# Kernel optimization log

Hardware: AMD Instinct MI355X
Metric: run time of the kernel (lower is better)

## Reference

```python
import jax, jax.numpy as jnp
import numpy as np

WS = 2
D = 128  # hidden_dim per direction
SCALE_X = float(np.sqrt(2.0))  # rescale=True, highway_bias=0 -> sqrt(1+exp(0))


def sru_bidir(x, W, wc, b, k):
    """Bidirectional single-layer SRU (sru lib, layer_norm=False, rescale=True).
    x: (L, N, din). Returns (L, N, 2*D)."""
    L, N, _ = x.shape
    U = (x @ W).reshape(L, N, 2, D, k)  # (L,N,dir,D,k)
    vf, vr = wc.reshape(2, 2, D)  # each (dir, D)
    bf, br = b.reshape(2, 2, D)
    # time-reverse the backward direction so one scan handles both
    U = jnp.concatenate([U[:, :, :1], U[::-1, :, 1:]], axis=2)
    if k == 4:
        xprime = U[..., 3]
    else:
        xp = x.reshape(L, N, 2, D)
        xprime = jnp.concatenate([xp[:, :, :1], xp[::-1, :, 1:]], axis=2) * SCALE_X

    def step(c, inp):
        u0, u1, u2, xpt = inp  # each (N,2,D)
        f = jax.nn.sigmoid(u1 + vf * c + bf)
        c = f * c + (1.0 - f) * u0
        r = jax.nn.sigmoid(u2 + vr * c + br)
        h = r * c + (1.0 - r) * xpt
        return c, h

    c0 = jnp.zeros((N, 2, D), dtype=x.dtype)
    _, H = jax.lax.scan(step, c0, (U[..., 0], U[..., 1], U[..., 2], xprime))
    # un-reverse backward direction outputs
    H = jnp.concatenate([H[:, :, :1], H[::-1, :, 1:]], axis=2)
    return H.reshape(L, N, 2 * D)


def setup_inputs() -> dict:
    key = jax.random.key(0)
    ks = jax.random.split(key, 6)
    B, C, Himg, Wimg = 8, 3, 224, 224
    F = WS * WS * C  # 12
    inp = {
        "x": jax.random.normal(ks[0], (B, C, Himg, Wimg), jnp.float32),
        "W1": jax.random.normal(ks[1], (F, 2 * D * 4), jnp.float32) * (1.0 / np.sqrt(F)),
        "wc1": jax.random.normal(ks[2], (2 * 2 * D,), jnp.float32) * 0.1,
        "b1": jnp.zeros((2 * 2 * D,), jnp.float32),
        "W2": jax.random.normal(ks[3], (2 * D, 2 * D * 3), jnp.float32) * (1.0 / np.sqrt(2 * D)),
        "wc2": jax.random.normal(ks[4], (2 * 2 * D,), jnp.float32) * 0.1,
        "b2": jnp.zeros((2 * 2 * D,), jnp.float32),
    }
    return inp


def reference(x, W1, wc1, b1, W2, wc2, b2):
    B, C, Himg, Wimg = x.shape
    Hp, Wp = Himg // WS, Wimg // WS
    F = WS * WS * C
    # get_valid_patches: (B, Hp, Wp, C*ws*ws) with (C, wh, ww) flatten order
    p = x.reshape(B, C, Hp, WS, Wp, WS).transpose(0, 2, 4, 1, 3, 5).reshape(B, Hp, Wp, F)
    # input_array = patches.permute(2,0,3,1) -> (Hp, B, Wp, F)
    # apply_one_direction on firstVRNN: merge Hp into batch, scan over Wp
    a1 = p.transpose(1, 0, 2, 3).reshape(Hp * B, Wp, F).transpose(1, 0, 2)  # (Wp, Hp*B, F)
    h1 = sru_bidir(a1, W1, wc1, b1, k=4)  # (Wp, Hp*B, 2D)
    h1 = h1.transpose(1, 0, 2).reshape(Hp, B, Wp, 2 * D)
    # vertical_results = out.permute(2,1,0,3) -> (Wp, B, Hp, 2D)
    v = h1.transpose(2, 1, 0, 3)
    # second direction: merge Wp into batch, scan over Hp
    a2 = v.reshape(Wp * B, Hp, 2 * D).transpose(1, 0, 2)  # (Hp, Wp*B, 2D)
    h2 = sru_bidir(a2, W2, wc2, b2, k=3)  # (Hp, Wp*B, 2D)
    h2 = h2.transpose(1, 0, 2).reshape(Wp, B, Hp, 2 * D)
    # feature_map.permute(1,3,2,0) -> (B, 2D, Hp, Wp)
    return h2.transpose(1, 3, 2, 0)
```

## Files before the change

### kernel.cpp

```cpp
#include <hip/hip_runtime.h>
#include <hip/hip_bf16.h>

typedef unsigned short ushort_t;
typedef unsigned int uint_t;

typedef __bf16 bf16x8 __attribute__((ext_vector_type(8)));
typedef float f32x4 __attribute__((ext_vector_type(4)));

__device__ __forceinline__ float bf2f(ushort_t u) {
    return __uint_as_float(((uint_t)u) << 16);
}
__device__ __forceinline__ ushort_t f2bf(float f) {
    uint_t x = __float_as_uint(f);
    uint_t r = (x + 0x7FFFu + ((x >> 16) & 1u)) >> 16;
    return (ushort_t)r;
}
__device__ __forceinline__ float sigmoidf_fast(float x) {
    return 1.0f / (1.0f + __expf(-x));
}

__global__ __launch_bounds__(256) void permute_w2(const float* __restrict__ W2,
                                                  ushort_t* __restrict__ W2t) {
    int i = blockIdx.x * 256 + threadIdx.x;
    int np = i >> 8;
    int k  = i & 255;
    int kk  = np >> 8;
    int rem = np & 255;
    int dir = rem >> 7;
    int d   = rem & 127;
    int oc = dir * 384 + d * 3 + kk;
    W2t[np * 256 + k] = f2bf(W2[k * 768 + oc]);
}

__global__ __launch_bounds__(256) void scan1(const float* __restrict__ x,
                                             const float* __restrict__ W1,
                                             const float* __restrict__ wc1,
                                             const float* __restrict__ b1,
                                             ushort_t* __restrict__ H1) {
    __shared__ float patch[112 * 12];
    const int n1 = blockIdx.x;
    const int hp = n1 >> 3, b = n1 & 7;
    const int tid = threadIdx.x;

    for (int e = tid; e < 1344; e += 256) {
        int c = e / 448;
        int rem = e % 448;
        int wh = rem / 224;
        int pos = rem % 224;
        float v = x[((b * 3 + c) * 224 + (2 * hp + wh)) * 224 + pos];
        patch[(pos >> 1) * 12 + c * 4 + wh * 2 + (pos & 1)] = v;
    }

    float4 w[12];
    const float4* W1v = (const float4*)W1;
#pragma unroll
    for (int j = 0; j < 12; ++j) w[j] = W1v[j * 256 + tid];

    const float vf = wc1[tid],       vr = wc1[256 + tid];
    const float bfv = b1[tid],       brv = b1[256 + tid];
    const int dir = tid >> 7;

    __syncthreads();

    float cst = 0.0f;
    for (int t = 0; t < 112; ++t) {
        const int tt = dir ? (111 - t) : t;
        const float4* pp = (const float4*)(patch + tt * 12);
        float4 p0 = pp[0], p1 = pp[1], p2 = pp[2];
        float pj[12] = {p0.x, p0.y, p0.z, p0.w, p1.x, p1.y, p1.z, p1.w,
                        p2.x, p2.y, p2.z, p2.w};
        float u0 = 0.f, u1 = 0.f, u2 = 0.f, u3 = 0.f;
#pragma unroll
        for (int j = 0; j < 12; ++j) {
            float pv = pj[j];
            u0 = fmaf(w[j].x, pv, u0);
            u1 = fmaf(w[j].y, pv, u1);
            u2 = fmaf(w[j].z, pv, u2);
            u3 = fmaf(w[j].w, pv, u3);
        }
        float f = sigmoidf_fast(u1 + vf * cst + bfv);
        cst = f * cst + (1.0f - f) * u0;
        float r = sigmoidf_fast(u2 + vr * cst + brv);
        float h = r * cst + (1.0f - r) * u3;
        H1[((size_t)(hp * 112 + tt) * 8 + b) * 256 + tid] = f2bf(h);
    }
}

__global__ __launch_bounds__(256) void gemm2(const ushort_t* __restrict__ A,
                                             const ushort_t* __restrict__ Bt,
                                             ushort_t* __restrict__ Cc) {
    __shared__ ushort_t As[128 * 32];
    __shared__ ushort_t Bs[128 * 32];
    const int m0 = blockIdx.y * 128;
    const int n0 = blockIdx.x * 128;
    const int tid = threadIdx.x;
    const int w = tid >> 6, lane = tid & 63;
    const int wm = w >> 1, wn = w & 1;
    const int lr = lane >> 2;
    const int lc = (lane & 3) * 8;
    const int ln16 = lane & 15;
    const int k8 = (lane >> 4) * 8;

    f32x4 acc[4][4] = {};

    for (int kb = 0; kb < 256; kb += 32) {
        if (kb) __syncthreads();
#pragma unroll
        for (int q = 0; q < 2; ++q) {
            int r = w * 32 + q * 16;
            const ushort_t* gA = A + (size_t)(m0 + r + lr) * 256 + kb + lc;
            __builtin_amdgcn_global_load_lds(
                (const __attribute__((address_space(1))) uint_t*)gA,
                (__attribute__((address_space(3))) uint_t*)(As + r * 32), 16, 0, 0);
            const ushort_t* gB = Bt + (size_t)(n0 + r + lr) * 256 + kb + lc;
            __builtin_amdgcn_global_load_lds(
                (const __attribute__((address_space(1))) uint_t*)gB,
                (__attribute__((address_space(3))) uint_t*)(Bs + r * 32), 16, 0, 0);
        }
        __syncthreads();

        bf16x8 af[4], bf[4];
#pragma unroll
        for (int i = 0; i < 4; ++i) {
            int ra = wm * 64 + i * 16 + ln16;
            af[i] = *(const bf16x8*)(As + ra * 32 + k8);
            int rb = wn * 64 + i * 16 + ln16;
            bf[i] = *(const bf16x8*)(Bs + rb * 32 + k8);
        }
#pragma unroll
        for (int i = 0; i < 4; ++i)
#pragma unroll
            for (int j = 0; j < 4; ++j)
                acc[i][j] = __builtin_amdgcn_mfma_f32_16x16x32_bf16(
                    af[i], bf[j], acc[i][j], 0, 0, 0);
    }

    const int rq = (lane >> 4) * 4;
#pragma unroll
    for (int i = 0; i < 4; ++i)
#pragma unroll
        for (int j = 0; j < 4; ++j)
#pragma unroll
            for (int r = 0; r < 4; ++r) {
                int gm = m0 + wm * 64 + i * 16 + rq + r;
                int gn = n0 + wn * 64 + j * 16 + ln16;
                Cc[(size_t)gm * 768 + gn] = f2bf(acc[i][j][r]);
            }
}

__global__ __launch_bounds__(256) void scan2(const ushort_t* __restrict__ U2,
                                             const ushort_t* __restrict__ H1,
                                             const float* __restrict__ wc2,
                                             const float* __restrict__ b2,
                                             float* __restrict__ H2) {
    const int n2 = blockIdx.x;
    const int wp = n2 >> 3, b = n2 & 7;
    const int tid = threadIdx.x;
    const int dir = tid >> 7;
    const float vf = wc2[tid],  vr = wc2[256 + tid];
    const float bfv = b2[tid],  brv = b2[256 + tid];
    const float SCALE_X = 1.41421356237309515f;

    float cst = 0.0f;
    for (int t = 0; t < 112; ++t) {
        const int tt = dir ? (111 - t) : t;
        const size_t m = (size_t)(tt * 112 + wp) * 8 + b;
        const ushort_t* u = U2 + m * 768;
        float u0 = bf2f(u[tid]);
        float u1 = bf2f(u[256 + tid]);
        float u2 = bf2f(u[512 + tid]);
        float xp = bf2f(H1[m * 256 + tid]) * SCALE_X;
        float f = sigmoidf_fast(u1 + vf * cst + bfv);
        cst = f * cst + (1.0f - f) * u0;
        float r = sigmoidf_fast(u2 + vr * cst + brv);
        H2[m * 256 + tid] = r * cst + (1.0f - r) * xp;
    }
}

__global__ __launch_bounds__(256) void transpose_out(const float* __restrict__ H2,
                                                     float* __restrict__ out) {
    __shared__ float tile[112 * 65];
    const int bid = blockIdx.x;
    const int cchunk = bid & 3;
    const int hp = (bid >> 2) % 112;
    const int b = bid / (4 * 112);
    const int tid = threadIdx.x;
    const int ch0 = cchunk * 64;

    for (int i = tid; i < 112 * 64; i += 256) {
        int wp = i >> 6;
        int c = i & 63;
        tile[wp * 65 + c] = H2[((size_t)(hp * 112 + wp) * 8 + b) * 256 + ch0 + c];
    }
    __syncthreads();
    for (int i = tid; i < 64 * 112; i += 256) {
        int c = i / 112;
        int wp = i % 112;
        out[((size_t)(b * 256 + ch0 + c) * 112 + hp) * 112 + wp] = tile[wp * 65 + c];
    }
}

extern "C" void kernel_launch(void* const* d_in, const int* in_sizes, int n_in,
                              void* d_out, int out_size, void* d_ws, size_t ws_size,
                              hipStream_t stream) {
    const float* x   = (const float*)d_in[0];
    const float* W1  = (const float*)d_in[1];
    const float* wc1 = (const float*)d_in[2];
    const float* b1  = (const float*)d_in[3];
    const float* W2  = (const float*)d_in[4];
    const float* wc2 = (const float*)d_in[5];
    const float* b2  = (const float*)d_in[6];
    float* out = (float*)d_out;

    char* ws = (char*)d_ws;
    ushort_t* H1  = (ushort_t*)(ws);
    ushort_t* U2  = (ushort_t*)(ws + 51380224);
    ushort_t* W2t = (ushort_t*)(ws + 51380224 + 154140672);
    float*    H2  = (float*)(ws + 51380224 + 154140672 + 393216);

    permute_w2<<<768, 256, 0, stream>>>(W2, W2t);
    scan1<<<896, 256, 0, stream>>>(x, W1, wc1, b1, H1);
    gemm2<<<dim3(6, 784), 256, 0, stream>>>(H1, W2t, U2);
    scan2<<<896, 256, 0, stream>>>(U2, H1, wc2, b2, H2);
    transpose_out<<<8 * 112 * 4, 256, 0, stream>>>(H2, out);
}
```

Before: 381.0 us.

## Store GEMM outputs channel-planar so scan2 writes final layout directly

scan1 now writes H1 in batch-major order. gemm2 writes U2 into per-gate planes laid out (b, channel, position), and a new xp_plane kernel transposes the scaled H1 into a fourth plane. scan2 is remapped so each thread owns one (channel, wp) column and writes the final NCHW output directly, with a one-step prefetch. This removes the separate H2 buffer and the transpose_out pass. The cost is an extra transpose kernel, scattered 8-byte stores from the GEMM epilogue, and many scan2 lanes idle because 112 of 128 wp slots are used.

```diff
diff --git a/kernel.cpp b/kernel.cpp
--- a/kernel.cpp
+++ b/kernel.cpp
@@ -18,6 +18,9 @@
 __device__ __forceinline__ float sigmoidf_fast(float x) {
     return 1.0f / (1.0f + __expf(-x));
 }
+
+#define PP 12544
+#define PLANE 25690112ULL
 
 __global__ __launch_bounds__(256) void permute_w2(const float* __restrict__ W2,
                                                   ushort_t* __restrict__ W2t) {
@@ -36,7 +39,7 @@
                                              const float* __restrict__ W1,
                                              const float* __restrict__ wc1,
                                              const float* __restrict__ b1,
-                                             ushort_t* __restrict__ H1) {
+                                             ushort_t* __restrict__ H1a) {
     __shared__ float patch[112 * 12];
     const int n1 = blockIdx.x;
     const int hp = n1 >> 3, b = n1 & 7;
@@ -82,17 +85,50 @@
         cst = f * cst + (1.0f - f) * u0;
         float r = sigmoidf_fast(u2 + vr * cst + brv);
         float h = r * cst + (1.0f - r) * u3;
-        H1[((size_t)(hp * 112 + tt) * 8 + b) * 256 + tid] = f2bf(h);
+        H1a[((size_t)b * PP + hp * 112 + tt) * 256 + tid] = f2bf(h);
+    }
+}
+
+__global__ __launch_bounds__(256) void xp_plane(const ushort_t* __restrict__ H1a,
+                                                ushort_t* __restrict__ U2t) {
+    __shared__ ushort_t tile[64 * 66];
+    const int pt = blockIdx.x;
+    const int ct = blockIdx.y;
+    const int b  = blockIdx.z;
+    const int p0 = pt * 64, ch0 = ct * 64;
+    const int tid = threadIdx.x;
+    const float SCALE_X = 1.41421356237309515f;
+
+#pragma unroll
+    for (int rep = 0; rep < 16; ++rep) {
+        int idx = rep * 256 + tid;
+        int pl = idx >> 6;
+        int cl = idx & 63;
+        float v = bf2f(H1a[((size_t)b * PP + p0 + pl) * 256 + ch0 + cl]);
+        tile[pl * 66 + cl] = f2bf(v * SCALE_X);
+    }
+    __syncthreads();
+#pragma unroll
+    for (int rep = 0; rep < 16; ++rep) {
+        int idx = rep * 256 + tid;
+        int cl = idx >> 6;
+        int pl = idx & 63;
+        U2t[3 * PLANE + ((size_t)b * 256 + ch0 + cl) * PP + p0 + pl] =
+            tile[pl * 66 + cl];
     }
 }
 
 __global__ __launch_bounds__(256) void gemm2(const ushort_t* __restrict__ A,
                                              const ushort_t* __restrict__ Bt,
-                                             ushort_t* __restrict__ Cc) {
+                                             ushort_t* __restrict__ U2t) {
     __shared__ ushort_t As[128 * 32];
     __shared__ ushort_t Bs[128 * 32];
     const int m0 = blockIdx.y * 128;
+    const int bb = blockIdx.y / 98;
+    const int p0 = (blockIdx.y % 98) * 128;
     const int n0 = blockIdx.x * 128;
+    const int kidx = n0 >> 8;
+    const int ch0  = n0 & 255;
     const int tid = threadIdx.x;
     const int w = tid >> 6, lane = tid & 63;
     const int wm = w >> 1, wn = w & 1;
@@ -122,10 +158,8 @@
         bf16x8 af[4], bf[4];
 #pragma unroll
         for (int i = 0; i < 4; ++i) {
-            int ra = wm * 64 + i * 16 + ln16;
-            af[i] = *(const bf16x8*)(As + ra * 32 + k8);
-            int rb = wn * 64 + i * 16 + ln16;
-            bf[i] = *(const bf16x8*)(Bs + rb * 32 + k8);
+            af[i] = *(const bf16x8*)(As + (wm * 64 + i * 16 + ln16) * 32 + k8);
+            bf[i] = *(const bf16x8*)(Bs + (wn * 64 + i * 16 + ln16) * 32 + k8);
         }
 #pragma unroll
         for (int i = 0; i < 4; ++i)
@@ -136,67 +170,69 @@
     }
 
     const int rq = (lane >> 4) * 4;
-#pragma unroll
-    for (int i = 0; i < 4; ++i)
-#pragma unroll
-        for (int j = 0; j < 4; ++j)
-#pragma unroll
-            for (int r = 0; r < 4; ++r) {
-                int gm = m0 + wm * 64 + i * 16 + rq + r;
-                int gn = n0 + wn * 64 + j * 16 + ln16;
-                Cc[(size_t)gm * 768 + gn] = f2bf(acc[i][j][r]);
-            }
-}
-
-__global__ __launch_bounds__(256) void scan2(const ushort_t* __restrict__ U2,
-                                             const ushort_t* __restrict__ H1,
+    const size_t planeBase = (size_t)kidx * PLANE + (size_t)(bb * 256 + ch0) * PP;
+#pragma unroll
+    for (int i = 0; i < 4; ++i) {
+        int p = p0 + wm * 64 + i * 16 + rq;
+#pragma unroll
+        for (int j = 0; j < 4; ++j) {
+            int ch_l = wn * 64 + j * 16 + ln16;
+            ushort4 v;
+            v.x = f2bf(acc[i][j][0]);
+            v.y = f2bf(acc[i][j][1]);
+            v.z = f2bf(acc[i][j][2]);
+            v.w = f2bf(acc[i][j][3]);
+            *(ushort4*)(U2t + planeBase + (size_t)ch_l * PP + p) = v;
+        }
+    }
+}
+
+__global__ __launch_bounds__(256) void scan2(const ushort_t* __restrict__ U2t,
                                              const float* __restrict__ wc2,
                                              const float* __restrict__ b2,
-                                             float* __restrict__ H2) {
-    const int n2 = blockIdx.x;
-    const int wp = n2 >> 3, b = n2 & 7;
-    const int tid = threadIdx.x;
-    const int dir = tid >> 7;
-    const float vf = wc2[tid],  vr = wc2[256 + tid];
-    const float bfv = b2[tid],  brv = b2[256 + tid];
-    const float SCALE_X = 1.41421356237309515f;
+                                             float* __restrict__ out) {
+    const int cb = blockIdx.x;
+    const int b  = blockIdx.y;
+    const int tid = threadIdx.x;
+    const int ch = cb * 2 + (tid >> 7);
+    const int wp = tid & 127;
+    if (wp >= 112) return;
+    const int dir = ch >> 7;
+
+    const float vf = wc2[ch],  vr = wc2[256 + ch];
+    const float bfv = b2[ch],  brv = b2[256 + ch];
+
+    const int tt0 = dir ? 111 : 0;
+    const long dstep = dir ? -112 : 112;
+    const long ostep = dir ? -112 : 112;
+
+    long off  = (long)((size_t)(b * 256 + ch) * PP) + tt0 * 112 + wp;
+    long oOff = (long)((size_t)(b * 256 + ch) * 112 + tt0) * 112 + wp;
+
+    const ushort_t* P = U2t;
+    ushort_t a0 = P[off];
+    ushort_t a1 = P[PLANE + off];
+    ushort_t a2 = P[2 * PLANE + off];
+    ushort_t a3 = P[3 * PLANE + off];
 
     float cst = 0.0f;
     for (int t = 0; t < 112; ++t) {
-        const int tt = dir ? (111 - t) : t;
-        const size_t m = (size_t)(tt * 112 + wp) * 8 + b;
-        const ushort_t* u = U2 + m * 768;
-        float u0 = bf2f(u[tid]);
-        float u1 = bf2f(u[256 + tid]);
-        float u2 = bf2f(u[512 + tid]);
-        float xp = bf2f(H1[m * 256 + tid]) * SCALE_X;
+        long noff = off + ((t < 111) ? dstep : 0);
+        ushort_t n0 = P[noff];
+        ushort_t n1 = P[PLANE + noff];
+        ushort_t n2 = P[2 * PLANE + noff];
+        ushort_t n3 = P[3 * PLANE + noff];
+
+        float u0 = bf2f(a0), u1 = bf2f(a1), u2v = bf2f(a2);
+        float xp = bf2f(a3);
         float f = sigmoidf_fast(u1 + vf * cst + bfv);
         cst = f * cst + (1.0f - f) * u0;
-        float r = sigmoidf_fast(u2 + vr * cst + brv);
-        H2[m * 256 + tid] = r * cst + (1.0f - r) * xp;
-    }
-}
-
-__global__ __launch_bounds__(256) void transpose_out(const float* __restrict__ H2,
-                                                     float* __restrict__ out) {
-    __shared__ float tile[112 * 65];
-    const int bid = blockIdx.x;
-    const int cchunk = bid & 3;
-    const int hp = (bid >> 2) % 112;
-    const int b = bid / (4 * 112);
-    const int tid = threadIdx.x;
-    const int ch0 = cchunk * 64;
-
-    for (int i = tid; i < 112 * 64; i += 256) {
-        int wp = i >> 6;
-        int c = i & 63;
-        tile[wp * 65 + c] = H2[((size_t)(hp * 112 + wp) * 8 + b) * 256 + ch0 + c];
-    }
-    __syncthreads();
-    for (int i = tid; i < 64 * 112; i += 256) {
-        int c = i / 112;
-        int wp = i % 112;
-        out[((size_t)(b * 256 + ch0 + c) * 112 + hp) * 112 + wp] = tile[wp * 65 + c];
+        float r = sigmoidf_fast(u2v + vr * cst + brv);
+        out[oOff] = r * cst + (1.0f - r) * xp;
+
+        a0 = n0; a1 = n1; a2 = n2; a3 = n3;
+        off = noff;
+        oOff += ostep;
     }
 }
 
@@ -213,14 +249,13 @@
     float* out = (float*)d_out;
 
     char* ws = (char*)d_ws;
-    ushort_t* H1  = (ushort_t*)(ws);
-    ushort_t* U2  = (ushort_t*)(ws + 51380224);
-    ushort_t* W2t = (ushort_t*)(ws + 51380224 + 154140672);
-    float*    H2  = (float*)(ws + 51380224 + 154140672 + 393216);
+    ushort_t* H1a = (ushort_t*)(ws);
+    ushort_t* U2t = (ushort_t*)(ws + 51380224);
+    ushort_t* W2t = (ushort_t*)(ws + 51380224 + 205520896);
 
     permute_w2<<<768, 256, 0, stream>>>(W2, W2t);
-    scan1<<<896, 256, 0, stream>>>(x, W1, wc1, b1, H1);
-    gemm2<<<dim3(6, 784), 256, 0, stream>>>(H1, W2t, U2);
-    scan2<<<896, 256, 0, stream>>>(U2, H1, wc2, b2, H2);
-    transpose_out<<<8 * 112 * 4, 256, 0, stream>>>(H2, out);
-}
+    scan1<<<896, 256, 0, stream>>>(x, W1, wc1, b1, H1a);
+    xp_plane<<<dim3(196, 4, 8), 256, 0, stream>>>(H1a, U2t);
+    gemm2<<<dim3(6, 784), 256, 0, stream>>>(H1a, W2t, U2t);
+    scan2<<<dim3(128, 8), 256, 0, stream>>>(U2t, wc2, b2, out);
+}
```

After: 401.9 us. 5.5% more time.
